# Kernel optimization log

Measured on AMD Instinct MI355X. Metric: run time of the kernel, lower is better.

## Reference

```python
import jax, jax.numpy as jnp
import numpy as np
from jax import lax

H = 106      # hidden size
IN = 100     # input feature size
S = 512      # sequence length (time-major)
B = 256      # batch
N_REST = 10  # layers 2..6 of lstm1 (5) + all 5 layers of lstm2, all 106->106


def _lstm_layer(x, Wih, Whh, bih, bhh):
    """Single LSTM layer, PyTorch gate order (i, f, g, o). x: (S, B, in)."""
    # Precompute input contribution for all timesteps at once: (S, B, 4H)
    gx = jnp.einsum('sbi,gi->sbg', x, Wih) + bih + bhh

    def step(carry, g_t):
        h, c = carry
        g = g_t + h @ Whh.T                      # (B, 4H)
        i, f, gg, o = jnp.split(g, 4, axis=-1)
        i = jax.nn.sigmoid(i)
        f = jax.nn.sigmoid(f)
        gg = jnp.tanh(gg)
        o = jax.nn.sigmoid(o)
        c = f * c + i * gg
        h = o * jnp.tanh(c)
        return (h, c), h

    b = x.shape[1]
    h0 = jnp.zeros((b, H), x.dtype)
    c0 = jnp.zeros((b, H), x.dtype)
    _, ys = lax.scan(step, (h0, c0), gx)
    return ys  # (S, B, H)


def setup_inputs() -> dict:
    key = jax.random.key(0)
    ks = jax.random.split(key, 10)
    k = 1.0 / np.sqrt(H)  # PyTorch LSTM default uniform init bound
    u = lambda kk, shape: jax.random.uniform(kk, shape, jnp.float32, -k, k)

    noise = jax.random.normal(ks[0], (S, B, IN), jnp.float32)
    # First layer: input dim 100
    W_ih0 = u(ks[1], (4 * H, IN))
    W_hh0 = u(ks[2], (4 * H, H))
    b_ih0 = u(ks[3], (4 * H,))
    b_hh0 = u(ks[4], (4 * H,))
    # Remaining 10 layers: input dim 106, stacked
    W_ih = u(ks[5], (N_REST, 4 * H, H))
    W_hh = u(ks[6], (N_REST, 4 * H, H))
    b_ih = u(ks[7], (N_REST, 4 * H))
    b_hh = u(ks[8], (N_REST, 4 * H))
    return {"noise": noise, "W_ih0": W_ih0, "W_hh0": W_hh0, "b_ih0": b_ih0,
            "b_hh0": b_hh0, "W_ih": W_ih, "W_hh": W_hh, "b_ih": b_ih, "b_hh": b_hh}


def reference(noise, W_ih0, W_hh0, b_ih0, b_hh0, W_ih, W_hh, b_ih, b_hh):
    x = _lstm_layer(noise, W_ih0, W_hh0, b_ih0, b_hh0)

    def layer_step(xc, params):
        Wih, Whh, bih, bhh = params
        return _lstm_layer(xc, Wih, Whh, bih, bhh), None

    x, _ = lax.scan(layer_step, x, (W_ih, W_hh, b_ih, b_hh))
    return x  # (S, B, H)
```

## Files before the change

### kernel.cpp

```cpp
#include <hip/hip_runtime.h>
#include <cmath>


namespace {
constexpr int H = 106, G4 = 424, SEQ = 512, BB = 256, KIN0 = 100;
constexpr int UST = 264;
constexpr int GST = 436;
constexpr int NTHR = 896;
constexpr int RGN = 16;
constexpr int NLAYER = 11;
constexpr int RD = 8;
constexpr int REL = 56;
constexpr size_t CNT_STRIDE = 16;
constexpr size_t RING_OFF_B = 65536;
constexpr size_t RING_PER_L = (size_t)RD * BB * REL;

using f16x8 = __attribute__((ext_vector_type(8))) _Float16;
using f32x4 = __attribute__((ext_vector_type(4))) float;
typedef unsigned long long u64;

__device__ __forceinline__ u64 ald(const u64* p) {
    return __hip_atomic_load(p, __ATOMIC_RELAXED, __HIP_MEMORY_SCOPE_AGENT);
}
__device__ __forceinline__ void ast(u64* p, u64 v) {
    __hip_atomic_store(p, v, __ATOMIC_RELAXED, __HIP_MEMORY_SCOPE_AGENT);
}
__device__ __forceinline__ void spinc(const unsigned* p, unsigned tgt) {
    while (__hip_atomic_load(p, __ATOMIC_RELAXED, __HIP_MEMORY_SCOPE_AGENT) < tgt)
        __builtin_amdgcn_s_sleep(8);
}
__device__ __forceinline__ float fast_tanh(float x) {
    float t = __expf(2.0f * x);
    return 1.0f - 2.0f / (t + 1.0f);
}
__device__ __forceinline__ float act_gate(float g, bool istanh) {
    float s = istanh ? 2.0f * g : g;
    float r = 1.0f / (1.0f + __expf(-s));
    return istanh ? 2.0f * r - 1.0f : r;
}
__device__ __forceinline__ unsigned packh2(float a, float b) {
    unsigned lo = (unsigned)__builtin_bit_cast(unsigned short, (_Float16)a);
    unsigned hi = (unsigned)__builtin_bit_cast(unsigned short, (_Float16)b);
    return (hi << 16) | lo;
}

__global__ __launch_bounds__(NTHR)
__attribute__((amdgpu_waves_per_eu(4, 4)))
void lstm_wave(const float* __restrict__ noise,
               float* __restrict__ yout,
               unsigned* cnt, u64* ring,
               const float* __restrict__ W_ih0, const float* __restrict__ W_hh0,
               const float* __restrict__ b_ih0, const float* __restrict__ b_hh0,
               const float* __restrict__ W_ih,  const float* __restrict__ W_hh,
               const float* __restrict__ b_ih,  const float* __restrict__ b_hh)
{
    const int l = blockIdx.x / RGN;
    const int rg = blockIdx.x % RGN;
    const bool LAST = (l == NLAYER - 1);
    const int K_IN = (l == 0) ? KIN0 : H;

    const float* Wih = (l == 0) ? W_ih0 : W_ih + (size_t)(l - 1) * G4 * H;
    const float* Whh = (l == 0) ? W_hh0 : W_hh + (size_t)(l - 1) * G4 * H;
    const float* pbi = (l == 0) ? b_ih0 : b_ih + (size_t)(l - 1) * G4;
    const float* pbh = (l == 0) ? b_hh0 : b_hh + (size_t)(l - 1) * G4;

    unsigned* cons_my = cnt + (size_t)(l * RGN + rg) * CNT_STRIDE;
    unsigned* cons_in = cnt + (size_t)((l - 1) * RGN + rg) * CNT_STRIDE;
    u64* ring_in  = ring + (size_t)(l - 1) * RING_PER_L;
    u64* ring_out = ring + (size_t)l * RING_PER_L;

    __shared__ __align__(16) _Float16 su[16 * UST];
    __shared__ float gl[16 * GST];

    const int tid = threadIdx.x;
    const int w = tid >> 6, lane = tid & 63;
    const int l16 = lane & 15, kg = lane >> 4;
    const int lm = tid / 56, ld = tid % 56;

    f16x8 bf[2][8];
    float bias[2];
    #pragma unroll
    for (int t = 0; t < 2; ++t) {
        const int n = 16 * (2 * w + t) + l16;
        const bool valid = n < G4;
        const float* pwx = Wih + (size_t)(valid ? n : 0) * K_IN;
        const float* pwh = Whh + (size_t)(valid ? n : 0) * H;
        #pragma unroll
        for (int q = 0; q < 8; ++q) {
            f16x8 v;
            #pragma unroll
            for (int e = 0; e < 8; ++e) {
                const int k = 32 * q + 8 * kg + e;
                float f = 0.0f;
                if (valid) {
                    if (k < 128) { if (k < K_IN) f = pwx[k]; }
                    else { const int kh = k - 128; if (kh < H) f = pwh[kh]; }
                }
                v[e] = (_Float16)f;
            }
            bf[t][q] = v;
        }
        bias[t] = valid ? (pbi[n] + pbh[n]) : 0.0f;
    }

    for (int i = tid; i < 16 * (UST / 2); i += NTHR) ((unsigned*)su)[i] = 0;
    float c0 = 0.0f, c1 = 0.0f;
    __syncthreads();
    {
        unsigned xr = 0;
        if (l == 0) {
            if (ld < 50) {
                const float2 v = *(const float2*)(noise + ((size_t)rg * 16 + lm) * KIN0 + 2 * ld);
                xr = packh2(v.x, v.y);
            }
        } else {
            const u64* p = ring_in + ((size_t)0 * BB + rg * 16 + lm) * REL + ld;
            u64 v = ald(p);
            while ((unsigned)(v >> 32) != 1u) { __builtin_amdgcn_s_sleep(1); v = ald(p); }
            xr = (unsigned)v;
        }
        ((unsigned*)su)[lm * 132 + ld] = xr;
    }
    __syncthreads();

    const _Float16* abase = su + (size_t)l16 * UST + 8 * kg;
    const int um = tid / 53, up = tid % 53;

    for (int s = 0; s < SEQ; ++s) {
        u64 v = 0; unsigned xr = 0;
        const bool wantx = (s + 1 < SEQ);
        const u64* pin = ring_in + ((size_t)((s + 1) % RD) * BB + rg * 16 + lm) * REL + ld;
        if (wantx) {
            if (l == 0) {
                if (ld < 50) {
                    const float2 t = *(const float2*)(noise + ((size_t)(s + 1) * BB + rg * 16 + lm) * KIN0 + 2 * ld);
                    xr = packh2(t.x, t.y);
                }
            } else {
                v = ald(pin);
            }
        }
        if (tid == 0 && !LAST && s >= RD) spinc(cons_my, (unsigned)(s - RD + 2));

        f32x4 acc[2] = {{0, 0, 0, 0}, {0, 0, 0, 0}};
        #pragma unroll
        for (int q = 0; q < 4; ++q) {
            const f16x8 a = *(const f16x8*)(abase + 32 * q);
            acc[0] = __builtin_amdgcn_mfma_f32_16x16x32_f16(a, bf[0][q], acc[0], 0, 0, 0);
            acc[1] = __builtin_amdgcn_mfma_f32_16x16x32_f16(a, bf[1][q], acc[1], 0, 0, 0);
        }
        __syncthreads();

        #pragma unroll
        for (int q = 4; q < 8; ++q) {
            const f16x8 a = *(const f16x8*)(abase + 32 * q);
            acc[0] = __builtin_amdgcn_mfma_f32_16x16x32_f16(a, bf[0][q], acc[0], 0, 0, 0);
            acc[1] = __builtin_amdgcn_mfma_f32_16x16x32_f16(a, bf[1][q], acc[1], 0, 0, 0);
        }
        #pragma unroll
        for (int t = 0; t < 2; ++t) {
            const int n = 16 * (2 * w + t) + l16;
            if (n < G4) {
                const bool istanh = (n >= 2 * H) && (n < 3 * H);
                #pragma unroll
                for (int r = 0; r < 4; ++r)
                    gl[(4 * kg + r) * GST + n] = act_gate(acc[t][r] + bias[t], istanh);
            }
        }
        if (wantx) {
            if (l > 0) {
                const unsigned expt = (unsigned)(s + 2);
                while ((unsigned)(v >> 32) != expt) { __builtin_amdgcn_s_sleep(1); v = ald(pin); }
                xr = (unsigned)v;
            }
            ((unsigned*)su)[lm * 132 + ld] = xr;
        }
        __syncthreads();

        if (tid < 848) {
            const float* gm = gl + um * GST;
            const float i0 = gm[2 * up],         i1 = gm[2 * up + 1];
            const float f0 = gm[H + 2 * up],     f1 = gm[H + 2 * up + 1];
            const float g0 = gm[2 * H + 2 * up], g1 = gm[2 * H + 2 * up + 1];
            const float o0 = gm[3 * H + 2 * up], o1 = gm[3 * H + 2 * up + 1];
            c0 = fmaf(f0, c0, i0 * g0);
            c1 = fmaf(f1, c1, i1 * g1);
            const float h0 = o0 * fast_tanh(c0);
            const float h1 = o1 * fast_tanh(c1);
            const unsigned hw = packh2(h0, h1);
            ((unsigned*)su)[um * 132 + 64 + up] = hw;
            if (LAST) {
                *(float2*)(yout + ((size_t)s * BB + rg * 16 + um) * H + 2 * up) =
                    make_float2(h0, h1);
            } else {
                ast(ring_out + ((size_t)(s % RD) * BB + rg * 16 + um) * REL + up,
                    ((u64)(unsigned)(s + 1) << 32) | hw);
            }
        } else if (!LAST) {
            const int t2 = tid - 848, m = t2 / 3, dd = t2 % 3;
            ast(ring_out + ((size_t)(s % RD) * BB + rg * 16 + m) * REL + 53 + dd,
                (u64)(unsigned)(s + 1) << 32);
        }
        __syncthreads();

        if (tid == 0 && l > 0 && s + 1 < SEQ)
            __hip_atomic_store(cons_in, (unsigned)(s + 2),
                               __ATOMIC_RELAXED, __HIP_MEMORY_SCOPE_AGENT);
    }
}
}

extern "C" void kernel_launch(void* const* d_in, const int* in_sizes, int n_in,
                              void* d_out, int out_size, void* d_ws, size_t ws_size,
                              hipStream_t stream) {
    const float* noise = (const float*)d_in[0];
    const float* W_ih0 = (const float*)d_in[1];
    const float* W_hh0 = (const float*)d_in[2];
    const float* b_ih0 = (const float*)d_in[3];
    const float* b_hh0 = (const float*)d_in[4];
    const float* W_ih  = (const float*)d_in[5];
    const float* W_hh  = (const float*)d_in[6];
    const float* b_ih  = (const float*)d_in[7];
    const float* b_hh  = (const float*)d_in[8];

    const size_t clear_bytes = RING_OFF_B + (size_t)NLAYER * RING_PER_L * sizeof(u64);
    hipMemsetAsync(d_ws, 0, clear_bytes, stream);

    unsigned* cnt = (unsigned*)d_ws;
    u64* ring = (u64*)((char*)d_ws + RING_OFF_B);

    lstm_wave<<<dim3(NLAYER * RGN), dim3(NTHR), 0, stream>>>(
        noise, (float*)d_out, cnt, ring,
        W_ih0, W_hh0, b_ih0, b_hh0, W_ih, W_hh, b_ih, b_hh);
}
```

Before: 1.476 ms.

## Split waves into recurrent and input-projection roles with double-buffered precompute

Restructures the per-layer block so 7 waves compute only the recurrent h·Whh MFMA plus the fused gate and cell update in registers. The other 7 waves precompute the next timestep's x·Wih projection into a double-buffered shared array, which takes input work off the serial recurrence path. The inter-layer ring changes from 64-bit to 32-bit entries, each holding a 16-bit step tag and one fp16 value. The ring depth doubles, consumer-credit polling runs every 8 steps, and activations use hardware exp2 and reciprocal intrinsics. The risks are more shared memory, 16-bit tag wraparound, and a goto-based control flow whose barriers must match across the two roles.

New measurement: 1.861 ms. +26.0%, slower.

```diff
diff --git a/kernel.cpp b/kernel.cpp
--- a/kernel.cpp
+++ b/kernel.cpp
@@ -3,52 +3,49 @@
 
 
 namespace {
-constexpr int H = 106, G4 = 424, SEQ = 512, BB = 256, KIN0 = 100;
-constexpr int UST = 264;
-constexpr int GST = 436;
-constexpr int NTHR = 896;
-constexpr int RGN = 16;
-constexpr int NLAYER = 11;
-constexpr int RD = 8;
-constexpr int REL = 56;
+constexpr int H = 106, SEQ = 512, BB = 256, KIN0 = 100;
+constexpr int NTHR = 896, RGN = 16, NLAYER = 11, RD = 16, RROW = 112;
 constexpr size_t CNT_STRIDE = 16;
 constexpr size_t RING_OFF_B = 65536;
-constexpr size_t RING_PER_L = (size_t)RD * BB * REL;
+constexpr size_t RING_PER_L = (size_t)RD * BB * RROW;
 
 using f16x8 = __attribute__((ext_vector_type(8))) _Float16;
 using f32x4 = __attribute__((ext_vector_type(4))) float;
-typedef unsigned long long u64;
-
-__device__ __forceinline__ u64 ald(const u64* p) {
+
+__device__ __forceinline__ unsigned aldu(const unsigned* p) {
     return __hip_atomic_load(p, __ATOMIC_RELAXED, __HIP_MEMORY_SCOPE_AGENT);
 }
-__device__ __forceinline__ void ast(u64* p, u64 v) {
+__device__ __forceinline__ void astu(unsigned* p, unsigned v) {
     __hip_atomic_store(p, v, __ATOMIC_RELAXED, __HIP_MEMORY_SCOPE_AGENT);
 }
 __device__ __forceinline__ void spinc(const unsigned* p, unsigned tgt) {
-    while (__hip_atomic_load(p, __ATOMIC_RELAXED, __HIP_MEMORY_SCOPE_AGENT) < tgt)
-        __builtin_amdgcn_s_sleep(8);
-}
-__device__ __forceinline__ float fast_tanh(float x) {
-    float t = __expf(2.0f * x);
-    return 1.0f - 2.0f / (t + 1.0f);
-}
-__device__ __forceinline__ float act_gate(float g, bool istanh) {
-    float s = istanh ? 2.0f * g : g;
-    float r = 1.0f / (1.0f + __expf(-s));
-    return istanh ? 2.0f * r - 1.0f : r;
-}
-__device__ __forceinline__ unsigned packh2(float a, float b) {
-    unsigned lo = (unsigned)__builtin_bit_cast(unsigned short, (_Float16)a);
-    unsigned hi = (unsigned)__builtin_bit_cast(unsigned short, (_Float16)b);
-    return (hi << 16) | lo;
-}
-
-__global__ __launch_bounds__(NTHR)
-__attribute__((amdgpu_waves_per_eu(4, 4)))
+    while (aldu(p) < tgt) __builtin_amdgcn_s_sleep(8);
+}
+__device__ __forceinline__ float fexp2(float x) {
+#if __has_builtin(__builtin_amdgcn_exp2f)
+    return __builtin_amdgcn_exp2f(x);
+#else
+    return __expf(x * 0.6931471806f);
+#endif
+}
+__device__ __forceinline__ float frcp(float x) {
+#if __has_builtin(__builtin_amdgcn_rcpf)
+    return __builtin_amdgcn_rcpf(x);
+#else
+    return 1.0f / x;
+#endif
+}
+__device__ __forceinline__ float fsig(float x) {
+    return frcp(1.0f + fexp2(-1.44269504f * x));
+}
+__device__ __forceinline__ float ftanh(float x) {
+    return fmaf(2.0f, frcp(1.0f + fexp2(-2.88539008f * x)), -1.0f);
+}
+
+__global__ __launch_bounds__(NTHR, 3)
 void lstm_wave(const float* __restrict__ noise,
                float* __restrict__ yout,
-               unsigned* cnt, u64* ring,
+               unsigned* cnt, unsigned* ring,
                const float* __restrict__ W_ih0, const float* __restrict__ W_hh0,
                const float* __restrict__ b_ih0, const float* __restrict__ b_hh0,
                const float* __restrict__ W_ih,  const float* __restrict__ W_hh,
@@ -59,153 +56,208 @@
     const bool LAST = (l == NLAYER - 1);
     const int K_IN = (l == 0) ? KIN0 : H;
 
-    const float* Wih = (l == 0) ? W_ih0 : W_ih + (size_t)(l - 1) * G4 * H;
-    const float* Whh = (l == 0) ? W_hh0 : W_hh + (size_t)(l - 1) * G4 * H;
-    const float* pbi = (l == 0) ? b_ih0 : b_ih + (size_t)(l - 1) * G4;
-    const float* pbh = (l == 0) ? b_hh0 : b_hh + (size_t)(l - 1) * G4;
+    const float* Wih = (l == 0) ? W_ih0 : W_ih + (size_t)(l - 1) * 4 * H * H;
+    const float* Whh = (l == 0) ? W_hh0 : W_hh + (size_t)(l - 1) * 4 * H * H;
+    const float* pbi = (l == 0) ? b_ih0 : b_ih + (size_t)(l - 1) * 4 * H;
+    const float* pbh = (l == 0) ? b_hh0 : b_hh + (size_t)(l - 1) * 4 * H;
 
     unsigned* cons_my = cnt + (size_t)(l * RGN + rg) * CNT_STRIDE;
     unsigned* cons_in = cnt + (size_t)((l - 1) * RGN + rg) * CNT_STRIDE;
-    u64* ring_in  = ring + (size_t)(l - 1) * RING_PER_L;
-    u64* ring_out = ring + (size_t)l * RING_PER_L;
-
-    __shared__ __align__(16) _Float16 su[16 * UST];
-    __shared__ float gl[16 * GST];
+    unsigned* ring_in  = ring + (size_t)(l - 1) * RING_PER_L;
+    unsigned* ring_out = ring + (size_t)l * RING_PER_L;
+
+    __shared__ __align__(16) float axb[2][448 * 20];
+    __shared__ __align__(16) _Float16 sx[2][16 * 136];
+    __shared__ __align__(16) _Float16 sh[16 * 136];
 
     const int tid = threadIdx.x;
-    const int w = tid >> 6, lane = tid & 63;
+    const int wid = tid >> 6, lane = tid & 63;
     const int l16 = lane & 15, kg = lane >> 4;
-    const int lm = tid / 56, ld = tid % 56;
-
-    f16x8 bf[2][8];
-    float bias[2];
+    const bool hrole = (wid < 7);
+    const int wg = hrole ? wid : wid - 7;
+    const int jh = 16 * wg + l16;
+    const bool jvalid = (jh < H);
+
+    f16x8 bf[4][4];
+    float bias[4] = {0.f, 0.f, 0.f, 0.f};
     #pragma unroll
-    for (int t = 0; t < 2; ++t) {
-        const int n = 16 * (2 * w + t) + l16;
-        const bool valid = n < G4;
-        const float* pwx = Wih + (size_t)(valid ? n : 0) * K_IN;
-        const float* pwh = Whh + (size_t)(valid ? n : 0) * H;
-        #pragma unroll
-        for (int q = 0; q < 8; ++q) {
+    for (int g = 0; g < 4; ++g) {
+        const int n = g * H + (jvalid ? jh : 0);
+        const float* pw = hrole ? (Whh + (size_t)n * H) : (Wih + (size_t)n * K_IN);
+        const int kmax = hrole ? H : K_IN;
+        #pragma unroll
+        for (int q = 0; q < 4; ++q) {
             f16x8 v;
             #pragma unroll
             for (int e = 0; e < 8; ++e) {
                 const int k = 32 * q + 8 * kg + e;
-                float f = 0.0f;
-                if (valid) {
-                    if (k < 128) { if (k < K_IN) f = pwx[k]; }
-                    else { const int kh = k - 128; if (kh < H) f = pwh[kh]; }
-                }
-                v[e] = (_Float16)f;
-            }
-            bf[t][q] = v;
-        }
-        bias[t] = valid ? (pbi[n] + pbh[n]) : 0.0f;
-    }
-
-    for (int i = tid; i < 16 * (UST / 2); i += NTHR) ((unsigned*)su)[i] = 0;
-    float c0 = 0.0f, c1 = 0.0f;
+                v[e] = (_Float16)((jvalid && k < kmax) ? pw[k] : 0.0f);
+            }
+            bf[g][q] = v;
+        }
+        if (hrole && jvalid) bias[g] = pbi[n] + pbh[n];
+    }
+
+    for (int i = tid; i < 2 * 1088 + 1088; i += NTHR) {
+        if (i < 2 * 1088) ((unsigned*)sx)[i] = 0;
+        else ((unsigned*)sh)[i - 2 * 1088] = 0;
+    }
+    float c[4] = {0.f, 0.f, 0.f, 0.f};
+
+    int m_[4], col_[4];
+    const unsigned* pb_[4];
+    const float* nb_[4];
+    if (!hrole) {
+        #pragma unroll
+        for (int e = 0; e < 4; ++e) {
+            const int flat = (tid - 448) + 448 * e;
+            m_[e] = flat / RROW;
+            col_[e] = flat % RROW;
+            pb_[e] = ring_in + (size_t)(rg * 16 + m_[e]) * RROW + col_[e];
+            nb_[e] = noise + (size_t)(rg * 16 + m_[e]) * 100 + col_[e];
+        }
+    }
     __syncthreads();
-    {
-        unsigned xr = 0;
-        if (l == 0) {
-            if (ld < 50) {
-                const float2 v = *(const float2*)(noise + ((size_t)rg * 16 + lm) * KIN0 + 2 * ld);
-                xr = packh2(v.x, v.y);
+
+    if (!hrole) {
+        #pragma unroll
+        for (int e = 0; e < 4; ++e) {
+            _Float16 val = (_Float16)0.0f;
+            if (l == 0) {
+                if (col_[e] < 100) val = (_Float16)nb_[e][0];
+            } else if (col_[e] < H) {
+                unsigned v = aldu(pb_[e]);
+                while ((v >> 16) != 1u) { __builtin_amdgcn_s_sleep(1); v = aldu(pb_[e]); }
+                val = __builtin_bit_cast(_Float16, (unsigned short)(v & 0xffffu));
+            }
+            sx[0][m_[e] * 136 + col_[e]] = val;
+        }
+    }
+    __syncthreads();
+
+    unsigned vcur[4] = {0, 0, 0, 0};
+    float npre[4] = {0.f, 0.f, 0.f, 0.f};
+    if (!hrole) {
+        f32x4 ax[4] = {{0,0,0,0},{0,0,0,0},{0,0,0,0},{0,0,0,0}};
+        const _Float16* ar = &sx[0][l16 * 136 + 8 * kg];
+        #pragma unroll
+        for (int q = 0; q < 4; ++q) {
+            const f16x8 a = *(const f16x8*)(ar + 32 * q);
+            #pragma unroll
+            for (int g = 0; g < 4; ++g)
+                ax[g] = __builtin_amdgcn_mfma_f32_16x16x32_f16(a, bf[g][q], ax[g], 0, 0, 0);
+        }
+        float* ab = &axb[0][(tid - 448) * 20];
+        #pragma unroll
+        for (int g = 0; g < 4; ++g) *(f32x4*)(ab + 4 * g) = ax[g];
+        #pragma unroll
+        for (int e = 0; e < 4; ++e) {
+            if (l == 0) { if (col_[e] < 100) npre[e] = nb_[e][(size_t)1 * BB * 100]; }
+            else if (col_[e] < H) vcur[e] = aldu(pb_[e] + ((size_t)(1 & (RD - 1)) * BB * RROW));
+        }
+    }
+    __syncthreads();
+
+    for (int s = 0; s < SEQ; ++s) {
+        const bool wantx = (s + 1 < SEQ);
+        if (!hrole) {
+            if (tid == 512 && !LAST && s >= RD && (s & 7) == 0)
+                spinc(cons_my, (unsigned)(s - 6));
+            if (wantx) {
+                #pragma unroll
+                for (int e = 0; e < 4; ++e) {
+                    _Float16 val = (_Float16)0.0f;
+                    if (l == 0) {
+                        if (col_[e] < 100) val = (_Float16)npre[e];
+                    } else if (col_[e] < H) {
+                        const unsigned expt = (unsigned)(s + 2);
+                        unsigned v = vcur[e];
+                        const unsigned* pin = pb_[e] + ((size_t)((s + 1) & (RD - 1)) * BB * RROW);
+                        while ((v >> 16) != expt) { __builtin_amdgcn_s_sleep(1); v = aldu(pin); }
+                        val = __builtin_bit_cast(_Float16, (unsigned short)(v & 0xffffu));
+                    }
+                    sx[(s + 1) & 1][m_[e] * 136 + col_[e]] = val;
+                }
             }
         } else {
-            const u64* p = ring_in + ((size_t)0 * BB + rg * 16 + lm) * REL + ld;
-            u64 v = ald(p);
-            while ((unsigned)(v >> 32) != 1u) { __builtin_amdgcn_s_sleep(1); v = ald(p); }
-            xr = (unsigned)v;
-        }
-        ((unsigned*)su)[lm * 132 + ld] = xr;
-    }
-    __syncthreads();
-
-    const _Float16* abase = su + (size_t)l16 * UST + 8 * kg;
-    const int um = tid / 53, up = tid % 53;
-
-    for (int s = 0; s < SEQ; ++s) {
-        u64 v = 0; unsigned xr = 0;
-        const bool wantx = (s + 1 < SEQ);
-        const u64* pin = ring_in + ((size_t)((s + 1) % RD) * BB + rg * 16 + lm) * REL + ld;
-        if (wantx) {
-            if (l == 0) {
-                if (ld < 50) {
-                    const float2 t = *(const float2*)(noise + ((size_t)(s + 1) * BB + rg * 16 + lm) * KIN0 + 2 * ld);
-                    xr = packh2(t.x, t.y);
-                }
-            } else {
-                v = ald(pin);
-            }
-        }
-        if (tid == 0 && !LAST && s >= RD) spinc(cons_my, (unsigned)(s - RD + 2));
-
-        f32x4 acc[2] = {{0, 0, 0, 0}, {0, 0, 0, 0}};
-        #pragma unroll
-        for (int q = 0; q < 4; ++q) {
-            const f16x8 a = *(const f16x8*)(abase + 32 * q);
-            acc[0] = __builtin_amdgcn_mfma_f32_16x16x32_f16(a, bf[0][q], acc[0], 0, 0, 0);
-            acc[1] = __builtin_amdgcn_mfma_f32_16x16x32_f16(a, bf[1][q], acc[1], 0, 0, 0);
+            f32x4 acc[4];
+            const float* ab = &axb[s & 1][tid * 20];
+            #pragma unroll
+            for (int g = 0; g < 4; ++g) acc[g] = *(const f32x4*)(ab + 4 * g);
+            const _Float16* ar = &sh[l16 * 136 + 8 * kg];
+            #pragma unroll
+            for (int q = 0; q < 4; ++q) {
+                const f16x8 a = *(const f16x8*)(ar + 32 * q);
+                #pragma unroll
+                for (int g = 0; g < 4; ++g)
+                    acc[g] = __builtin_amdgcn_mfma_f32_16x16x32_f16(a, bf[g][q], acc[g], 0, 0, 0);
+            }
+            float ga[4][4];
+            #pragma unroll
+            for (int g = 0; g < 4; ++g)
+                #pragma unroll
+                for (int r = 0; r < 4; ++r) {
+                    const float v = acc[g][r] + bias[g];
+                    ga[g][r] = (g == 2) ? ftanh(v) : fsig(v);
+                }
+            #pragma unroll
+            for (int r = 0; r < 4; ++r) {
+                c[r] = fmaf(ga[1][r], c[r], ga[0][r] * ga[2][r]);
+                const float hv = ga[3][r] * ftanh(c[r]);
+                const _Float16 h16 = (_Float16)hv;
+                ga[0][r] = hv;
+                ga[1][r] = __builtin_bit_cast(unsigned short, h16) * 1.0f;
+                ga[2][r] = 0.f;
+                (void)h16;
+            }
+            __syncthreads();
+            #pragma unroll
+            for (int r = 0; r < 4; ++r) {
+                const float hv = ga[0][r];
+                const _Float16 h16 = (_Float16)hv;
+                sh[(4 * kg + r) * 136 + jh] = h16;
+                if (jvalid) {
+                    if (LAST) {
+                        yout[((size_t)s * BB + rg * 16 + 4 * kg + r) * H + jh] = hv;
+                    } else {
+                        astu(ring_out + (size_t)(s & (RD - 1)) * BB * RROW
+                                      + (size_t)(rg * 16 + 4 * kg + r) * RROW + jh,
+                             ((unsigned)(s + 1) << 16) |
+                             (unsigned)__builtin_bit_cast(unsigned short, h16));
+                    }
+                }
+            }
+            goto after_b1;
         }
         __syncthreads();
-
-        #pragma unroll
-        for (int q = 4; q < 8; ++q) {
-            const f16x8 a = *(const f16x8*)(abase + 32 * q);
-            acc[0] = __builtin_amdgcn_mfma_f32_16x16x32_f16(a, bf[0][q], acc[0], 0, 0, 0);
-            acc[1] = __builtin_amdgcn_mfma_f32_16x16x32_f16(a, bf[1][q], acc[1], 0, 0, 0);
-        }
-        #pragma unroll
-        for (int t = 0; t < 2; ++t) {
-            const int n = 16 * (2 * w + t) + l16;
-            if (n < G4) {
-                const bool istanh = (n >= 2 * H) && (n < 3 * H);
-                #pragma unroll
-                for (int r = 0; r < 4; ++r)
-                    gl[(4 * kg + r) * GST + n] = act_gate(acc[t][r] + bias[t], istanh);
-            }
-        }
-        if (wantx) {
-            if (l > 0) {
-                const unsigned expt = (unsigned)(s + 2);
-                while ((unsigned)(v >> 32) != expt) { __builtin_amdgcn_s_sleep(1); v = ald(pin); }
-                xr = (unsigned)v;
-            }
-            ((unsigned*)su)[lm * 132 + ld] = xr;
+after_b1:
+        if (!hrole) {
+            if (wantx) {
+                f32x4 ax[4] = {{0,0,0,0},{0,0,0,0},{0,0,0,0},{0,0,0,0}};
+                const _Float16* ar = &sx[(s + 1) & 1][l16 * 136 + 8 * kg];
+                #pragma unroll
+                for (int q = 0; q < 4; ++q) {
+                    const f16x8 a = *(const f16x8*)(ar + 32 * q);
+                    #pragma unroll
+                    for (int g = 0; g < 4; ++g)
+                        ax[g] = __builtin_amdgcn_mfma_f32_16x16x32_f16(a, bf[g][q], ax[g], 0, 0, 0);
+                }
+                float* ab = &axb[(s + 1) & 1][(tid - 448) * 20];
+                #pragma unroll
+                for (int g = 0; g < 4; ++g) *(f32x4*)(ab + 4 * g) = ax[g];
+                if (s + 2 < SEQ) {
+                    #pragma unroll
+                    for (int e = 0; e < 4; ++e) {
+                        if (l == 0) { if (col_[e] < 100) npre[e] = nb_[e][(size_t)(s + 2) * BB * 100]; }
+                        else if (col_[e] < H)
+                            vcur[e] = aldu(pb_[e] + ((size_t)((s + 2) & (RD - 1)) * BB * RROW));
+                    }
+                }
+            }
+            if (tid == 448 && l > 0 && wantx)
+                astu(cons_in, (unsigned)(s + 2));
         }
         __syncthreads();
-
-        if (tid < 848) {
-            const float* gm = gl + um * GST;
-            const float i0 = gm[2 * up],         i1 = gm[2 * up + 1];
-            const float f0 = gm[H + 2 * up],     f1 = gm[H + 2 * up + 1];
-            const float g0 = gm[2 * H + 2 * up], g1 = gm[2 * H + 2 * up + 1];
-            const float o0 = gm[3 * H + 2 * up], o1 = gm[3 * H + 2 * up + 1];
-            c0 = fmaf(f0, c0, i0 * g0);
-            c1 = fmaf(f1, c1, i1 * g1);
-            const float h0 = o0 * fast_tanh(c0);
-            const float h1 = o1 * fast_tanh(c1);
-            const unsigned hw = packh2(h0, h1);
-            ((unsigned*)su)[um * 132 + 64 + up] = hw;
-            if (LAST) {
-                *(float2*)(yout + ((size_t)s * BB + rg * 16 + um) * H + 2 * up) =
-                    make_float2(h0, h1);
-            } else {
-                ast(ring_out + ((size_t)(s % RD) * BB + rg * 16 + um) * REL + up,
-                    ((u64)(unsigned)(s + 1) << 32) | hw);
-            }
-        } else if (!LAST) {
-            const int t2 = tid - 848, m = t2 / 3, dd = t2 % 3;
-            ast(ring_out + ((size_t)(s % RD) * BB + rg * 16 + m) * REL + 53 + dd,
-                (u64)(unsigned)(s + 1) << 32);
-        }
-        __syncthreads();
-
-        if (tid == 0 && l > 0 && s + 1 < SEQ)
-            __hip_atomic_store(cons_in, (unsigned)(s + 2),
-                               __ATOMIC_RELAXED, __HIP_MEMORY_SCOPE_AGENT);
     }
 }
 }
@@ -223,11 +275,11 @@
     const float* b_ih  = (const float*)d_in[7];
     const float* b_hh  = (const float*)d_in[8];
 
-    const size_t clear_bytes = RING_OFF_B + (size_t)NLAYER * RING_PER_L * sizeof(u64);
+    const size_t clear_bytes = RING_OFF_B + (size_t)10 * RING_PER_L * sizeof(unsigned);
     hipMemsetAsync(d_ws, 0, clear_bytes, stream);
 
     unsigned* cnt = (unsigned*)d_ws;
-    u64* ring = (u64*)((char*)d_ws + RING_OFF_B);
+    unsigned* ring = (unsigned*)((char*)d_ws + RING_OFF_B);
 
     lstm_wave<<<dim3(NLAYER * RGN), dim3(NTHR), 0, stream>>>(
         noise, (float*)d_out, cnt, ring,
```
